# Optimization experiments

Hardware: AMD Instinct MI355X
Metric: run time of the kernel (lower is better)

## Reference

```python
import jax, jax.numpy as jnp
import numpy as np

# Config constants (MLAConfig)
B, S = 1, 2048                 # batch, context_len (prefill: seq == context_len)
H = 16                         # num_heads
DN, DR, DV = 128, 64, 128      # qk_nope_head_dim, qk_rope_head_dim, v_head_dim
QL, C = 1536, 512              # q_lora_rank, kv_lora_rank
BLK = 128                      # fp8 dequant block size
MAX_CACHE = 4096
SOFTMAX_SCALE = 1.0 / np.sqrt(DN + DR)  # 1/sqrt(192)
NEG_INF = -10000.0


def gen_rope(n_total, head_size):
    # theta_j = 10000^{-2j/d}; idx_theta[i, 0, :] = [i*theta, i*theta] (repeated halves)
    theta = 1.0 / (10000.0 ** (jnp.arange(0, head_size, 2, dtype=jnp.float32) / head_size))
    idx = jnp.outer(jnp.arange(n_total, dtype=jnp.float32), theta)  # (N, d/2)
    return jnp.tile(idx[:, None, :], (1, 1, 2))                     # (N, 1, d)


def fp8_dequant(x, s, block=BLK):
    # Block-wise dequant: x (M,N) * per-(block x block) scale s (M/b, N/b).
    M, N = x.shape
    m, n = M // block, N // block  # shapes chosen divisible by block -> no padding
    return (x.reshape(m, block, n, block) * s[:, None, :, None]).reshape(M, N)


def apply_rope(x, cos, sin):
    # x: (B*S, heads, d). Interleaved RoPE: de-interleave pairs into halves,
    # then x*cos + rotate_half(x)*sin with cos/sin (B*S, 1, d).
    bs, h, d = x.shape
    x = x.reshape(bs, h, d // 2, 2).transpose(0, 1, 3, 2).reshape(bs, h, d)
    rot = jnp.concatenate([-x[..., d // 2:], x[..., :d // 2]], axis=-1)
    return x * cos + rot * sin


def setup_inputs() -> dict:
    key = jax.random.key(0)
    ks = jax.random.split(key, 9)
    WUQ = jax.random.normal(ks[0], (H * (DN + DR), QL), dtype=jnp.float32)
    WUKV = jax.random.normal(ks[1], (H * (DN + DV), C), dtype=jnp.float32)
    # positive, small block scales so attention logits stay well-conditioned
    WUQ_scale = 0.05 * jax.random.uniform(ks[2], (H * (DN + DR) // BLK, QL // BLK), dtype=jnp.float32)
    WUKV_scale = 0.05 * jax.random.uniform(ks[3], (H * (DN + DV) // BLK, C // BLK), dtype=jnp.float32)
    Q = jax.random.normal(ks[4], (B, S, QL), dtype=jnp.float32)
    KV = jax.random.normal(ks[5], (B, S, C), dtype=jnp.float32)
    PE = jax.random.normal(ks[6], (B, S, DR), dtype=jnp.float32)
    kv_cache = jax.random.normal(ks[7], (B, MAX_CACHE, C), dtype=jnp.float32)
    pe_cache = jax.random.normal(ks[8], (B, MAX_CACHE, DR), dtype=jnp.float32)
    idx_theta = gen_rope(B * S, DR)
    mask = jnp.triu(jnp.full((S, S), NEG_INF, dtype=jnp.float32), k=1)
    return {"WUQ": WUQ, "WUQ_scale": WUQ_scale, "WUKV": WUKV, "WUKV_scale": WUKV_scale,
            "Q": Q, "KV": KV, "PE": PE, "kv_cache": kv_cache, "pe_cache": pe_cache,
            "idx_theta": idx_theta, "mask": mask}


def reference(WUQ, WUQ_scale, WUKV, WUKV_scale, Q, KV, PE, kv_cache, pe_cache, idx_theta, mask):
    bsz, seqlen, _ = Q.shape
    # fp8 block-wise dequant of the low-rank up-projection weights
    WUQd = fp8_dequant(WUQ, WUQ_scale)
    WUKVd = fp8_dequant(WUKV, WUKV_scale)
    # Q up-projection from q_lora latent: (B*S, QL) @ (QL, H*(DN+DR))
    q = (Q.reshape(-1, QL) @ WUQd.T).reshape(bsz, seqlen, H, DN + DR)
    q_nope, q_pe = q[..., :DN], q[..., DN:]
    cos, sin = jnp.cos(idx_theta), jnp.sin(idx_theta)  # (B*S, 1, DR)
    q_pe = apply_rope(q_pe.reshape(bsz * seqlen, H, DR), cos, sin).reshape(bsz, seqlen, H, DR)
    k_pe = apply_rope(PE.reshape(bsz * seqlen, 1, DR), cos, sin).reshape(bsz, seqlen, DR)
    # absorbed low-rank K matrix: q_nope projected into the kv latent space
    W3 = WUKVd.reshape(H, DN + DV, C)
    q_lat = jnp.einsum('bshd,hdc->bshc', q_nope, W3[:, :DN])
    # continuous-cache prefill: write fresh latents into the cache, attend over them
    kv = kv_cache.at[:, :seqlen].set(KV)[:, :seqlen]   # (B, S, C)
    pe = pe_cache.at[:, :seqlen].set(k_pe)[:, :seqlen]  # (B, S, DR)
    scores = (jnp.einsum('bshc,btc->bsht', q_lat, kv)
              + jnp.einsum('bshr,btr->bsht', q_pe, pe)) * SOFTMAX_SCALE
    scores = scores + mask[None, :, None, :]
    attn = jax.nn.softmax(scores, axis=-1)
    x = jnp.einsum('bsht,btc->bshc', attn, kv)
    out = jnp.einsum('bshc,hdc->bshd', x, W3[:, DN:])  # V up-projection (absorbed)
    return out  # (B, S, H, DV)
```

## Files before the change

### kernel.cpp

```cpp
#include <hip/hip_runtime.h>

typedef __bf16 bf16_t;
typedef __attribute__((ext_vector_type(4))) __bf16 bf16x4;
typedef __attribute__((ext_vector_type(8))) __bf16 bf16x8;
typedef __attribute__((ext_vector_type(4))) float f32x4;

#define SOFTMAX_SCALE 0.07216878364870322f
#define NEG_MASK (-10000.0f)

__device__ __forceinline__ void async16(const bf16_t* g, bf16_t* l) {
  __builtin_amdgcn_global_load_lds(
      (const __attribute__((address_space(1))) unsigned int*)g,
      (__attribute__((address_space(3))) unsigned int*)l, 16, 0, 0);
}


__global__ void k_rope_tables(const float* __restrict__ idxt,
                              float* __restrict__ cost, float* __restrict__ sint) {
  int i = blockIdx.x * 256 + threadIdx.x;
  float a = idxt[i];
  cost[i] = cosf(a);
  sint[i] = sinf(a);
}

__global__ void k_dequant(const float* __restrict__ W, const float* __restrict__ S,
                          bf16_t* __restrict__ out, int cols, int scols) {
  int i = (blockIdx.x * 256 + threadIdx.x) * 4;
  int r = i / cols, c = i % cols;
  float s = S[(r >> 7) * scols + (c >> 7)];
  float4 w = *(const float4*)(W + i);
  out[i + 0] = (bf16_t)(w.x * s);
  out[i + 1] = (bf16_t)(w.y * s);
  out[i + 2] = (bf16_t)(w.z * s);
  out[i + 3] = (bf16_t)(w.w * s);
}

__global__ void k_wv1t(const bf16_t* __restrict__ Wd, bf16_t* __restrict__ Wt) {
  int i = blockIdx.x * 256 + threadIdx.x;
  int c = i & 511, d = (i >> 9) & 127, h = i >> 16;
  Wt[(h << 16) + (c << 7) + d] = Wd[((h << 8) + d) * 512 + c];
}

__global__ void k_f32_to_bf16(const float* __restrict__ in, bf16_t* __restrict__ out) {
  int i = (blockIdx.x * 256 + threadIdx.x) * 4;
  float4 v = *(const float4*)(in + i);
  out[i + 0] = (bf16_t)(v.x * SOFTMAX_SCALE);
  out[i + 1] = (bf16_t)(v.y * SOFTMAX_SCALE);
  out[i + 2] = (bf16_t)(v.z * SOFTMAX_SCALE);
  out[i + 3] = (bf16_t)(v.w * SOFTMAX_SCALE);
}

__global__ void k_k4(const float* __restrict__ KV, bf16_t* __restrict__ K4) {
  int i = blockIdx.x * 256 + threadIdx.x;
  int c2 = i & 15, t = i >> 4;
  int tt = t >> 6, k = t & 63;
  const float* src = KV + (size_t)t * 512 + c2 * 32;
  bf16_t* dst = K4 + (size_t)tt * 36864 + c2 * 2048 + k * 8;
#pragma unroll
  for (int sub = 0; sub < 4; ++sub) {
    float4 u = *(const float4*)(src + sub * 8);
    float4 v = *(const float4*)(src + sub * 8 + 4);
    bf16x8 o;
    o[0] = (bf16_t)u.x; o[1] = (bf16_t)u.y; o[2] = (bf16_t)u.z; o[3] = (bf16_t)u.w;
    o[4] = (bf16_t)v.x; o[5] = (bf16_t)v.y; o[6] = (bf16_t)v.z; o[7] = (bf16_t)v.w;
    *(bf16x8*)(dst + sub * 512) = o;
  }
}

__global__ void k_v4(const float* __restrict__ KV, bf16_t* __restrict__ V4) {
  int i = blockIdx.x * 256 + threadIdx.x;
  int c = i & 511, a = i >> 9;
  int t0 = a * 8, tt = t0 >> 6;
  int key0 = t0 & 63, kk2 = key0 >> 5, sub = (key0 >> 3) & 3;
  bf16x8 o;
#pragma unroll
  for (int j = 0; j < 8; ++j)
    o[j] = (bf16_t)KV[(size_t)(t0 + j) * 512 + c];
  *(bf16x8*)(V4 + (size_t)tt * 32768 + kk2 * 16384 + sub * 4096 + c * 8) = o;
}

__global__ void k_pe_rope(const float* __restrict__ PE, const float* __restrict__ cost,
                          const float* __restrict__ sint, bf16_t* __restrict__ K4) {
  int i = blockIdx.x * 256 + threadIdx.x;
  int t = i >> 5, j = i & 31;
  float e = PE[t * 64 + 2 * j], o = PE[t * 64 + 2 * j + 1];
  float c1 = cost[t * 64 + j], s1 = sint[t * 64 + j];
  float c2 = cost[t * 64 + 32 + j], s2 = sint[t * 64 + 32 + j];
  int tt = t >> 6, k = t & 63;
  bf16_t* base = K4 + (size_t)tt * 36864 + (j >> 3) * 512 + k * 8 + (j & 7);
  base[16 * 2048] = (bf16_t)(e * c1 - o * s1);
  base[17 * 2048] = (bf16_t)(o * c2 + e * s2);
}

__global__ void k_q_rope(const bf16_t* __restrict__ q, const float* __restrict__ cost,
                         const float* __restrict__ sint, bf16_t* __restrict__ qfull) {
  int i = blockIdx.x * 256 + threadIdx.x;
  int j = i & 31, h = (i >> 5) & 15, t = i >> 9;
  const bf16_t* src = q + t * 3072 + h * 192 + 128;
  float e = (float)src[2 * j], o = (float)src[2 * j + 1];
  float c1 = cost[t * 64 + j], s1 = sint[t * 64 + j];
  float c2 = cost[t * 64 + 32 + j], s2 = sint[t * 64 + 32 + j];
  bf16_t* dst = qfull + (size_t)h * 2048 * 576 + t * 576 + 512;
  dst[j]      = (bf16_t)(e * c1 - o * s1);
  dst[32 + j] = (bf16_t)(o * c2 + e * s2);
}

template <int OUT_F32>
__global__ __launch_bounds__(256) void k_gemm(
    const bf16_t* __restrict__ A, int lda, long saz,
    const bf16_t* __restrict__ B, int ldb, long sbz,
    void* __restrict__ Cv, int ldc, long scz, int K) {
  __shared__ __attribute__((aligned(16))) bf16_t At[128 * 64];
  __shared__ __attribute__((aligned(16))) bf16_t Bt[128 * 64];
  const int tid = threadIdx.x;
  const int lane = tid & 63;
  const int wv = tid >> 6;
  const int fr = lane & 15, fq = lane >> 4;
  const int wm = (wv & 1) * 64, wn = (wv >> 1) * 64;
  const int m0 = blockIdx.x * 128, n0 = blockIdx.y * 128;
  const bf16_t* Ab = A + (long)blockIdx.z * saz;
  const bf16_t* Bb = B + (long)blockIdx.z * sbz;

  f32x4 acc[4][4] = {};
  bf16x8 va[4], vb[4];
#pragma unroll
  for (int j = 0; j < 4; ++j) {
    int ch = tid + j * 256, ar = ch >> 3, ac = (ch & 7) * 8;
    va[j] = *(const bf16x8*)(Ab + (size_t)(m0 + ar) * lda + ac);
    vb[j] = *(const bf16x8*)(Bb + (size_t)(n0 + ar) * ldb + ac);
  }

  for (int k0 = 0; k0 < K; k0 += 64) {
    __syncthreads();
#pragma unroll
    for (int j = 0; j < 4; ++j) {
      int ch = tid + j * 256, ar = ch >> 3, c8 = ch & 7;
      *(bf16x8*)(At + ar * 64 + ((c8 ^ (ar & 7)) * 8)) = va[j];
      *(bf16x8*)(Bt + ar * 64 + ((c8 ^ (ar & 7)) * 8)) = vb[j];
    }
    __syncthreads();
    if (k0 + 64 < K) {
#pragma unroll
      for (int j = 0; j < 4; ++j) {
        int ch = tid + j * 256, ar = ch >> 3, ac = (ch & 7) * 8;
        va[j] = *(const bf16x8*)(Ab + (size_t)(m0 + ar) * lda + k0 + 64 + ac);
        vb[j] = *(const bf16x8*)(Bb + (size_t)(n0 + ar) * ldb + k0 + 64 + ac);
      }
    }
#pragma unroll
    for (int kk = 0; kk < 2; ++kk) {
      bf16x8 af[4], bfr[4];
#pragma unroll
      for (int m = 0; m < 4; ++m)
        af[m] = *(const bf16x8*)(At + (wm + m * 16 + fr) * 64 + (((kk * 4 + fq) ^ (fr & 7)) * 8));
#pragma unroll
      for (int n = 0; n < 4; ++n)
        bfr[n] = *(const bf16x8*)(Bt + (wn + n * 16 + fr) * 64 + (((kk * 4 + fq) ^ (fr & 7)) * 8));
#pragma unroll
      for (int m = 0; m < 4; ++m)
#pragma unroll
        for (int n = 0; n < 4; ++n)
          acc[m][n] = __builtin_amdgcn_mfma_f32_16x16x32_bf16(af[m], bfr[n], acc[m][n], 0, 0, 0);
    }
  }
#pragma unroll
  for (int m = 0; m < 4; ++m) {
    int row = m0 + wm + m * 16 + fq * 4;
#pragma unroll
    for (int n = 0; n < 4; ++n) {
      int col = n0 + wn + n * 16 + fr;
#pragma unroll
      for (int i = 0; i < 4; ++i) {
        if (OUT_F32)
          ((float*)Cv)[(long)blockIdx.z * scz + (size_t)(row + i) * ldc + col] = acc[m][n][i];
        else
          ((bf16_t*)Cv)[(long)blockIdx.z * scz + (size_t)(row + i) * ldc + col] = (bf16_t)acc[m][n][i];
      }
    }
  }
}

__global__ __attribute__((amdgpu_flat_work_group_size(512, 512),
                          amdgpu_waves_per_eu(2, 2)))
void k_attn(const bf16_t* __restrict__ qfull,
            const bf16_t* __restrict__ K4,
            const bf16_t* __restrict__ V4,
            bf16_t* __restrict__ X) {
  __shared__ __attribute__((aligned(16))) bf16_t Kt[18 * 2048];
  __shared__ __attribute__((aligned(16))) bf16_t Vt[2 * 16384];
  __shared__ __attribute__((aligned(16))) bf16_t P[64 * 64];
  __shared__ __attribute__((aligned(16))) bf16_t Qpe[8 * 512];
  __shared__ float lred[4][64];

  const int tid = threadIdx.x;
  const int lane = tid & 63;
  const int w = tid >> 6;
  const int fr = lane & 15, fq = lane >> 4;
  const int h = blockIdx.x & 15;
  const int qt = 31 - (blockIdx.x >> 4);
  const int nt = qt + 1;
  const int rg = w >> 2;
  const int kq = w & 3;

  const bf16_t* qh = qfull + (size_t)h * 2048 * 576;
  bf16_t* Xh = X + (size_t)h * 2048 * 512;

  {
    int row = tid >> 3, sub = tid & 7;
    bf16x8 v = *(const bf16x8*)(qh + (size_t)(qt * 64 + row) * 576 + 512 + sub * 8);
    *(bf16x8*)(Qpe + sub * 512 + row * 8) = v;
  }

  bf16x8 qa[2][16];
  {
    const bf16_t* qb = qh + (size_t)(qt * 64 + rg * 32) * 576;
#pragma unroll
    for (int mf = 0; mf < 2; ++mf)
#pragma unroll
      for (int kk = 0; kk < 16; ++kk)
        qa[mf][kk] = *(const bf16x8*)(qb + (mf * 16 + fr) * 576 + kk * 32 + fq * 8);
  }

#pragma unroll
  for (int i = 0; i < 9; ++i) {
    int ck = w + 8 * i;
    async16(K4 + ck * 512 + lane * 8, Kt + ck * 512 + lane * 8);
  }

  f32x4 acc[2][8] = {};
  float lreg[2] = {0.f, 0.f};

  for (int t = 0; t < nt; ++t) {
    __syncthreads();

    {
      const bf16_t* vsrc = V4 + (size_t)t * 32768;
#pragma unroll
      for (int i = 0; i < 8; ++i) {
        int cv = w + 8 * i;
        async16(vsrc + cv * 512 + lane * 8, Vt + cv * 512 + lane * 8);
      }
    }

    f32x4 s[2] = {};
    __builtin_amdgcn_s_setprio(1);
#pragma unroll
    for (int kk = 0; kk < 16; ++kk) {
      bf16x8 kf = *(const bf16x8*)(Kt + kk * 2048 + fq * 512 + (kq * 16 + fr) * 8);
      s[0] = __builtin_amdgcn_mfma_f32_16x16x32_bf16(kf, qa[0][kk], s[0], 0, 0, 0);
      s[1] = __builtin_amdgcn_mfma_f32_16x16x32_bf16(kf, qa[1][kk], s[1], 0, 0, 0);
    }
#pragma unroll
    for (int kk = 16; kk < 18; ++kk) {
      bf16x8 kf = *(const bf16x8*)(Kt + kk * 2048 + fq * 512 + (kq * 16 + fr) * 8);
      bf16x8 q0 = *(const bf16x8*)(Qpe + ((kk - 16) * 4 + fq) * 512 + (rg * 32 + fr) * 8);
      bf16x8 q1 = *(const bf16x8*)(Qpe + ((kk - 16) * 4 + fq) * 512 + (rg * 32 + 16 + fr) * 8);
      s[0] = __builtin_amdgcn_mfma_f32_16x16x32_bf16(kf, q0, s[0], 0, 0, 0);
      s[1] = __builtin_amdgcn_mfma_f32_16x16x32_bf16(kf, q1, s[1], 0, 0, 0);
    }
    __builtin_amdgcn_s_setprio(0);

    bool diag = (t == qt);
#pragma unroll
    for (int mf = 0; mf < 2; ++mf) {
      int qrow = rg * 32 + mf * 16 + fr;
      if (diag) {
#pragma unroll
        for (int i = 0; i < 4; ++i) {
          int kcol = kq * 16 + fq * 4 + i;
          if (kcol > qrow) s[mf][i] += NEG_MASK;
        }
      }
      float p0 = __expf(s[mf][0]);
      float p1 = __expf(s[mf][1]);
      float p2 = __expf(s[mf][2]);
      float p3 = __expf(s[mf][3]);
      bf16x4 pk;
      pk[0] = (bf16_t)p0; pk[1] = (bf16_t)p1; pk[2] = (bf16_t)p2; pk[3] = (bf16_t)p3;
      int chunk = (kq * 2 + (fq >> 1)) ^ (qrow & 7);
      *(bf16x4*)(P + qrow * 64 + chunk * 8 + (fq & 1) * 4) = pk;
      lreg[mf] += (p0 + p1) + (p2 + p3);
    }
    __syncthreads();

    if (t + 1 < nt) {
      const bf16_t* ksrc = K4 + (size_t)(t + 1) * 36864;
#pragma unroll
      for (int i = 0; i < 9; ++i) {
        int ck = w + 8 * i;
        async16(ksrc + ck * 512 + lane * 8, Kt + ck * 512 + lane * 8);
      }
    }

    __builtin_amdgcn_s_setprio(1);
#pragma unroll
    for (int kk2 = 0; kk2 < 2; ++kk2) {
      bf16x8 pa[2];
#pragma unroll
      for (int mf = 0; mf < 2; ++mf) {
        int qrow = rg * 32 + mf * 16 + fr;
        pa[mf] = *(const bf16x8*)(P + qrow * 64 + (((kk2 * 4 + fq) ^ (qrow & 7)) * 8));
      }
#pragma unroll
      for (int nf = 0; nf < 8; ++nf) {
        bf16x8 vb = *(const bf16x8*)(Vt + kk2 * 16384 + fq * 4096 + (kq * 128 + nf * 16 + fr) * 8);
        acc[0][nf] = __builtin_amdgcn_mfma_f32_16x16x32_bf16(pa[0], vb, acc[0][nf], 0, 0, 0);
        acc[1][nf] = __builtin_amdgcn_mfma_f32_16x16x32_bf16(pa[1], vb, acc[1][nf], 0, 0, 0);
      }
    }
    __builtin_amdgcn_s_setprio(0);
  }

#pragma unroll
  for (int mf = 0; mf < 2; ++mf) {
    float lw = lreg[mf];
    lw += __shfl_xor(lw, 16);
    lw += __shfl_xor(lw, 32);
    if (fq == 0) lred[kq][rg * 32 + mf * 16 + fr] = lw;
  }
  __syncthreads();

  {
    bf16_t* XT = Kt;
#pragma unroll
    for (int mf = 0; mf < 2; ++mf)
#pragma unroll
      for (int i = 0; i < 4; ++i) {
        int row = rg * 32 + mf * 16 + fq * 4 + i;
        float invl = 1.0f / ((lred[0][row] + lred[1][row]) + (lred[2][row] + lred[3][row]));
#pragma unroll
        for (int nf = 0; nf < 8; ++nf)
          XT[row * 512 + kq * 128 + nf * 16 + fr] = (bf16_t)(acc[mf][nf][i] * invl);
      }
  }
  __syncthreads();
#pragma unroll
  for (int it = 0; it < 8; ++it) {
    int id = tid + it * 512;
    int row = id >> 6, j = id & 63;
    *(bf16x8*)(Xh + (size_t)(qt * 64 + row) * 512 + j * 8) = *(const bf16x8*)(Kt + row * 512 + j * 8);
  }
}


extern "C" void kernel_launch(void* const* d_in, const int* in_sizes, int n_in,
                              void* d_out, int out_size, void* d_ws, size_t ws_size,
                              hipStream_t stream) {
  (void)in_sizes; (void)n_in; (void)out_size; (void)ws_size;
  const float* WUQ   = (const float*)d_in[0];
  const float* WUQs  = (const float*)d_in[1];
  const float* WUKV  = (const float*)d_in[2];
  const float* WUKVs = (const float*)d_in[3];
  const float* Q     = (const float*)d_in[4];
  const float* KV    = (const float*)d_in[5];
  const float* PE    = (const float*)d_in[6];
  const float* idxt  = (const float*)d_in[9];
  float* out = (float*)d_out;

  char* ws = (char*)d_ws;
  size_t off = 0;
  auto alloc = [&](size_t n) -> char* {
    char* p = ws + off;
    off += (n + 255) & ~(size_t)255;
    return p;
  };
  float*  cost  = (float*)alloc((size_t)2048 * 64 * 4);
  float*  sint  = (float*)alloc((size_t)2048 * 64 * 4);
  bf16_t* WUQd  = (bf16_t*)alloc((size_t)3072 * 1536 * 2);
  bf16_t* WUKVd = (bf16_t*)alloc((size_t)4096 * 512 * 2);
  bf16_t* Wv1t  = (bf16_t*)alloc((size_t)16 * 512 * 128 * 2);
  bf16_t* Qb    = (bf16_t*)alloc((size_t)2048 * 1536 * 2);
  bf16_t* qbuf  = (bf16_t*)alloc((size_t)2048 * 3072 * 2);
  bf16_t* K4    = (bf16_t*)alloc((size_t)32 * 36864 * 2);
  bf16_t* V4    = (bf16_t*)alloc((size_t)32 * 32768 * 2);
  bf16_t* qfull = (bf16_t*)alloc((size_t)16 * 2048 * 576 * 2);
  bf16_t* Xb    = (bf16_t*)alloc((size_t)16 * 2048 * 512 * 2);

  k_rope_tables<<<512, 256, 0, stream>>>(idxt, cost, sint);
  k_dequant<<<4608, 256, 0, stream>>>(WUQ, WUQs, WUQd, 1536, 12);
  k_dequant<<<2048, 256, 0, stream>>>(WUKV, WUKVs, WUKVd, 512, 4);
  k_wv1t<<<4096, 256, 0, stream>>>(WUKVd, Wv1t);
  k_f32_to_bf16<<<3072, 256, 0, stream>>>(Q, Qb);
  k_k4<<<128, 256, 0, stream>>>(KV, K4);
  k_v4<<<512, 256, 0, stream>>>(KV, V4);
  k_pe_rope<<<256, 256, 0, stream>>>(PE, cost, sint, K4);
  k_gemm<0><<<dim3(16, 24, 1), 256, 0, stream>>>(Qb, 1536, 0, WUQd, 1536, 0,
                                                 qbuf, 3072, 0, 1536);
  k_q_rope<<<4096, 256, 0, stream>>>(qbuf, cost, sint, qfull);
  k_gemm<0><<<dim3(16, 4, 16), 256, 0, stream>>>(qbuf, 3072, 192, Wv1t, 128, (long)512 * 128,
                                                 qfull, 576, (long)2048 * 576, 128);
  k_attn<<<dim3(512), dim3(512), 0, stream>>>(qfull, K4, V4, Xb);
  k_gemm<1><<<dim3(16, 1, 16), 256, 0, stream>>>(Xb, 512, (long)2048 * 512,
                                                 WUKVd + 128 * 512, 512, (long)256 * 512,
                                                 out, 2048, 128, 512);
}
```

Before: 211.6 us.

## Pre-tile Q and WUQ into MFMA-friendly layout and fold rope tables into kernels

Q and the dequantized WUQ are converted into a pre-tiled bf16 layout so a new specialized GEMM can stream contiguous 16 KB k-slices into LDS with double buffering. The separate cos/sin table kernel is dropped and cos/sin are computed inline from idx_theta, relying on the repeated-halves structure of the rope angles so the second half reuses the first half's values. This is meant to reduce the cost of the Q up-projection and remove one launch plus table traffic, at the price of extra trig work per thread and an assumption about the input angle structure.

```diff
diff --git a/kernel.cpp b/kernel.cpp
--- a/kernel.cpp
+++ b/kernel.cpp
@@ -14,14 +14,6 @@
       (__attribute__((address_space(3))) unsigned int*)l, 16, 0, 0);
 }
 
-
-__global__ void k_rope_tables(const float* __restrict__ idxt,
-                              float* __restrict__ cost, float* __restrict__ sint) {
-  int i = blockIdx.x * 256 + threadIdx.x;
-  float a = idxt[i];
-  cost[i] = cosf(a);
-  sint[i] = sinf(a);
-}
 
 __global__ void k_dequant(const float* __restrict__ W, const float* __restrict__ S,
                           bf16_t* __restrict__ out, int cols, int scols) {
@@ -35,19 +27,42 @@
   out[i + 3] = (bf16_t)(w.w * s);
 }
 
+__global__ void k_qa4(const float* __restrict__ Q, bf16_t* __restrict__ A4) {
+  int i = blockIdx.x * 256 + threadIdx.x;
+  int m = i & 127, sub = (i >> 7) & 3, r = i >> 9;
+  int kk = r % 48, mt = r / 48;
+  const float* src = Q + (size_t)(mt * 128 + m) * 1536 + kk * 32 + sub * 8;
+  float4 u = *(const float4*)src;
+  float4 v = *(const float4*)(src + 4);
+  bf16x8 o;
+  o[0] = (bf16_t)(u.x * SOFTMAX_SCALE); o[1] = (bf16_t)(u.y * SOFTMAX_SCALE);
+  o[2] = (bf16_t)(u.z * SOFTMAX_SCALE); o[3] = (bf16_t)(u.w * SOFTMAX_SCALE);
+  o[4] = (bf16_t)(v.x * SOFTMAX_SCALE); o[5] = (bf16_t)(v.y * SOFTMAX_SCALE);
+  o[6] = (bf16_t)(v.z * SOFTMAX_SCALE); o[7] = (bf16_t)(v.w * SOFTMAX_SCALE);
+  *(bf16x8*)(A4 + (size_t)i * 8) = o;
+}
+
+__global__ void k_wb4(const float* __restrict__ W, const float* __restrict__ S,
+                      bf16_t* __restrict__ B4) {
+  int i = blockIdx.x * 256 + threadIdx.x;
+  int m = i & 127, sub = (i >> 7) & 3, r = i >> 9;
+  int kk = r % 48, nt = r / 48;
+  float s = S[nt * 12 + (kk >> 2)];
+  const float* src = W + (size_t)(nt * 128 + m) * 1536 + kk * 32 + sub * 8;
+  float4 u = *(const float4*)src;
+  float4 v = *(const float4*)(src + 4);
+  bf16x8 o;
+  o[0] = (bf16_t)(u.x * s); o[1] = (bf16_t)(u.y * s);
+  o[2] = (bf16_t)(u.z * s); o[3] = (bf16_t)(u.w * s);
+  o[4] = (bf16_t)(v.x * s); o[5] = (bf16_t)(v.y * s);
+  o[6] = (bf16_t)(v.z * s); o[7] = (bf16_t)(v.w * s);
+  *(bf16x8*)(B4 + (size_t)i * 8) = o;
+}
+
 __global__ void k_wv1t(const bf16_t* __restrict__ Wd, bf16_t* __restrict__ Wt) {
   int i = blockIdx.x * 256 + threadIdx.x;
   int c = i & 511, d = (i >> 9) & 127, h = i >> 16;
   Wt[(h << 16) + (c << 7) + d] = Wd[((h << 8) + d) * 512 + c];
-}
-
-__global__ void k_f32_to_bf16(const float* __restrict__ in, bf16_t* __restrict__ out) {
-  int i = (blockIdx.x * 256 + threadIdx.x) * 4;
-  float4 v = *(const float4*)(in + i);
-  out[i + 0] = (bf16_t)(v.x * SOFTMAX_SCALE);
-  out[i + 1] = (bf16_t)(v.y * SOFTMAX_SCALE);
-  out[i + 2] = (bf16_t)(v.z * SOFTMAX_SCALE);
-  out[i + 3] = (bf16_t)(v.w * SOFTMAX_SCALE);
 }
 
 __global__ void k_k4(const float* __restrict__ KV, bf16_t* __restrict__ K4) {
@@ -79,30 +94,90 @@
   *(bf16x8*)(V4 + (size_t)tt * 32768 + kk2 * 16384 + sub * 4096 + c * 8) = o;
 }
 
-__global__ void k_pe_rope(const float* __restrict__ PE, const float* __restrict__ cost,
-                          const float* __restrict__ sint, bf16_t* __restrict__ K4) {
+__global__ void k_pe_rope(const float* __restrict__ PE, const float* __restrict__ idxt,
+                          bf16_t* __restrict__ K4) {
   int i = blockIdx.x * 256 + threadIdx.x;
   int t = i >> 5, j = i & 31;
+  float a = idxt[t * 64 + j];
+  float c1 = cosf(a), s1 = sinf(a);
   float e = PE[t * 64 + 2 * j], o = PE[t * 64 + 2 * j + 1];
-  float c1 = cost[t * 64 + j], s1 = sint[t * 64 + j];
-  float c2 = cost[t * 64 + 32 + j], s2 = sint[t * 64 + 32 + j];
   int tt = t >> 6, k = t & 63;
   bf16_t* base = K4 + (size_t)tt * 36864 + (j >> 3) * 512 + k * 8 + (j & 7);
   base[16 * 2048] = (bf16_t)(e * c1 - o * s1);
-  base[17 * 2048] = (bf16_t)(o * c2 + e * s2);
-}
-
-__global__ void k_q_rope(const bf16_t* __restrict__ q, const float* __restrict__ cost,
-                         const float* __restrict__ sint, bf16_t* __restrict__ qfull) {
+  base[17 * 2048] = (bf16_t)(o * c1 + e * s1);
+}
+
+__global__ void k_q_rope(const bf16_t* __restrict__ q, const float* __restrict__ idxt,
+                         bf16_t* __restrict__ qfull) {
   int i = blockIdx.x * 256 + threadIdx.x;
   int j = i & 31, h = (i >> 5) & 15, t = i >> 9;
+  float a = idxt[t * 64 + j];
+  float c1 = cosf(a), s1 = sinf(a);
   const bf16_t* src = q + t * 3072 + h * 192 + 128;
   float e = (float)src[2 * j], o = (float)src[2 * j + 1];
-  float c1 = cost[t * 64 + j], s1 = sint[t * 64 + j];
-  float c2 = cost[t * 64 + 32 + j], s2 = sint[t * 64 + 32 + j];
   bf16_t* dst = qfull + (size_t)h * 2048 * 576 + t * 576 + 512;
   dst[j]      = (bf16_t)(e * c1 - o * s1);
-  dst[32 + j] = (bf16_t)(o * c2 + e * s2);
+  dst[32 + j] = (bf16_t)(o * c1 + e * s1);
+}
+
+__global__ __launch_bounds__(256) void k_gemm2(const bf16_t* __restrict__ A4,
+                                               const bf16_t* __restrict__ B4,
+                                               bf16_t* __restrict__ C) {
+  __shared__ __attribute__((aligned(16))) bf16_t At[2][8192];
+  __shared__ __attribute__((aligned(16))) bf16_t Bt[2][8192];
+  const int tid = threadIdx.x;
+  const int lane = tid & 63;
+  const int wv = tid >> 6;
+  const int fr = lane & 15, fq = lane >> 4;
+  const int wm = (wv & 1) * 64, wn = (wv >> 1) * 64;
+  const bf16_t* Asrc = A4 + (size_t)blockIdx.x * 196608;
+  const bf16_t* Bsrc = B4 + (size_t)blockIdx.y * 196608;
+
+#define STAGE2(bufp, ks)                                              \
+  do {                                                                \
+    const bf16_t* as_ = Asrc + (size_t)(ks) * 8192;                   \
+    const bf16_t* bs_ = Bsrc + (size_t)(ks) * 8192;                   \
+    _Pragma("unroll") for (int i_ = 0; i_ < 4; ++i_) {                \
+      int c_ = tid + i_ * 256;                                        \
+      async16(as_ + c_ * 8, At[bufp] + c_ * 8);                       \
+      async16(bs_ + c_ * 8, Bt[bufp] + c_ * 8);                       \
+    }                                                                 \
+  } while (0)
+
+  f32x4 acc[4][4] = {};
+  STAGE2(0, 0);
+  for (int ks = 0; ks < 24; ++ks) {
+    int buf = ks & 1;
+    __syncthreads();
+    if (ks + 1 < 24) STAGE2(buf ^ 1, ks + 1);
+#pragma unroll
+    for (int kkl = 0; kkl < 2; ++kkl) {
+      bf16x8 af[4], bfr[4];
+#pragma unroll
+      for (int m = 0; m < 4; ++m)
+        af[m] = *(const bf16x8*)(At[buf] + kkl * 4096 + fq * 1024 + (wm + m * 16 + fr) * 8);
+#pragma unroll
+      for (int n = 0; n < 4; ++n)
+        bfr[n] = *(const bf16x8*)(Bt[buf] + kkl * 4096 + fq * 1024 + (wn + n * 16 + fr) * 8);
+#pragma unroll
+      for (int m = 0; m < 4; ++m)
+#pragma unroll
+        for (int n = 0; n < 4; ++n)
+          acc[m][n] = __builtin_amdgcn_mfma_f32_16x16x32_bf16(af[m], bfr[n], acc[m][n], 0, 0, 0);
+    }
+  }
+#undef STAGE2
+#pragma unroll
+  for (int m = 0; m < 4; ++m) {
+    int row = blockIdx.x * 128 + wm + m * 16 + fq * 4;
+#pragma unroll
+    for (int n = 0; n < 4; ++n) {
+      int col = blockIdx.y * 128 + wn + n * 16 + fr;
+#pragma unroll
+      for (int i = 0; i < 4; ++i)
+        C[(size_t)(row + i) * 3072 + col] = (bf16_t)acc[m][n][i];
+    }
+  }
 }
 
 template <int OUT_F32>
@@ -364,29 +439,25 @@
     off += (n + 255) & ~(size_t)255;
     return p;
   };
-  float*  cost  = (float*)alloc((size_t)2048 * 64 * 4);
-  float*  sint  = (float*)alloc((size_t)2048 * 64 * 4);
-  bf16_t* WUQd  = (bf16_t*)alloc((size_t)3072 * 1536 * 2);
+  bf16_t* A4    = (bf16_t*)alloc((size_t)2048 * 1536 * 2);
+  bf16_t* B4    = (bf16_t*)alloc((size_t)3072 * 1536 * 2);
   bf16_t* WUKVd = (bf16_t*)alloc((size_t)4096 * 512 * 2);
   bf16_t* Wv1t  = (bf16_t*)alloc((size_t)16 * 512 * 128 * 2);
-  bf16_t* Qb    = (bf16_t*)alloc((size_t)2048 * 1536 * 2);
   bf16_t* qbuf  = (bf16_t*)alloc((size_t)2048 * 3072 * 2);
   bf16_t* K4    = (bf16_t*)alloc((size_t)32 * 36864 * 2);
   bf16_t* V4    = (bf16_t*)alloc((size_t)32 * 32768 * 2);
   bf16_t* qfull = (bf16_t*)alloc((size_t)16 * 2048 * 576 * 2);
   bf16_t* Xb    = (bf16_t*)alloc((size_t)16 * 2048 * 512 * 2);
 
-  k_rope_tables<<<512, 256, 0, stream>>>(idxt, cost, sint);
-  k_dequant<<<4608, 256, 0, stream>>>(WUQ, WUQs, WUQd, 1536, 12);
   k_dequant<<<2048, 256, 0, stream>>>(WUKV, WUKVs, WUKVd, 512, 4);
+  k_wb4<<<2304, 256, 0, stream>>>(WUQ, WUQs, B4);
+  k_qa4<<<1536, 256, 0, stream>>>(Q, A4);
   k_wv1t<<<4096, 256, 0, stream>>>(WUKVd, Wv1t);
-  k_f32_to_bf16<<<3072, 256, 0, stream>>>(Q, Qb);
   k_k4<<<128, 256, 0, stream>>>(KV, K4);
   k_v4<<<512, 256, 0, stream>>>(KV, V4);
-  k_pe_rope<<<256, 256, 0, stream>>>(PE, cost, sint, K4);
-  k_gemm<0><<<dim3(16, 24, 1), 256, 0, stream>>>(Qb, 1536, 0, WUQd, 1536, 0,
-                                                 qbuf, 3072, 0, 1536);
-  k_q_rope<<<4096, 256, 0, stream>>>(qbuf, cost, sint, qfull);
+  k_pe_rope<<<256, 256, 0, stream>>>(PE, idxt, K4);
+  k_gemm2<<<dim3(16, 24), 256, 0, stream>>>(A4, B4, qbuf);
+  k_q_rope<<<4096, 256, 0, stream>>>(qbuf, idxt, qfull);
   k_gemm<0><<<dim3(16, 4, 16), 256, 0, stream>>>(qbuf, 3072, 192, Wv1t, 128, (long)512 * 128,
                                                  qfull, 576, (long)2048 * 576, 128);
   k_attn<<<dim3(512), dim3(512), 0, stream>>>(qfull, K4, V4, Xb);
```

After: 222.5 us. 5.2% more time.
